# Kernel tuning notes

Hardware: AMD Instinct MI355X
Metric: run time of the kernel (lower is better)

The kernel has to match this reference:

```python
import jax, jax.numpy as jnp
import numpy as np
import math

H = 16
D_ATTN = 64
D_MID = 64
D_X = 1024
D_Z = 1024
D_OUT = 1024
B = 2
L_X = 2048
L_Z = 2048
MINUS_INFINITY = -1000000.0

def _xavier(key, shape):
    fan_in, fan_out = shape
    limit = math.sqrt(6.0 / (fan_in + fan_out))
    return jax.random.uniform(key, shape, jnp.float32, -limit, limit)

def setup_inputs() -> dict:
    key = jax.random.key(0)
    ks = jax.random.split(key, 8)
    primary = jax.random.normal(ks[0], (B, L_X, D_X), jnp.float32)
    context = jax.random.normal(ks[1], (B, L_Z, D_Z), jnp.float32)
    padding_mask = jnp.ones((B, L_Z), jnp.int32)
    # causal attention mask (b, l_x, l_z)
    attention_mask = jnp.broadcast_to(
        jnp.tril(jnp.ones((L_X, L_Z), jnp.int32))[None], (B, L_X, L_Z))
    W_qs = _xavier(ks[2], (D_X, H * D_ATTN))
    W_ks = _xavier(ks[3], (D_Z, H * D_ATTN))
    W_vs = _xavier(ks[4], (D_Z, H * D_MID))
    W_o = _xavier(ks[5], (H * D_MID, D_OUT))
    b_o = jnp.zeros((D_OUT,), jnp.float32)
    return {"primary": primary, "context": context,
            "padding_mask": padding_mask, "attention_mask": attention_mask,
            "W_qs": W_qs, "W_ks": W_ks, "W_vs": W_vs, "W_o": W_o, "b_o": b_o}

def reference(primary, context, padding_mask, attention_mask, W_qs, W_ks, W_vs, W_o, b_o):
    b, l_x, _ = primary.shape
    l_z = context.shape[1]
    # QKV projections, split into heads (head-major columns)
    q = (primary @ W_qs).reshape(b, l_x, H, D_ATTN).transpose(0, 2, 1, 3)  # (b,h,l_x,d_attn)
    k = (context @ W_ks).reshape(b, l_z, H, D_ATTN).transpose(0, 2, 1, 3)  # (b,h,l_z,d_attn)
    v = (context @ W_vs).reshape(b, l_z, H, D_MID).transpose(0, 2, 1, 3)   # (b,h,l_z,d_mid)
    scores = jnp.einsum('bhxd,bhzd->bhxz', q, k) / math.sqrt(D_ATTN)
    # combined mask: attention_mask AND padding_mask, broadcast over heads
    mask = (attention_mask * padding_mask[:, None, :])[:, None]  # (b,1,l_x,l_z)
    scores = jnp.where(mask == 0, MINUS_INFINITY, scores)
    attn = jax.nn.softmax(scores, axis=-1)
    out = jnp.einsum('bhxz,bhzm->bhxm', attn, v)  # (b,h,l_x,d_mid)
    out = out.transpose(0, 2, 1, 3).reshape(b, l_x, H * D_MID)
    return out @ W_o + b_o
```

## Files before the change

kernel.cpp:

```cpp
#include <hip/hip_runtime.h>

#define NB 2
#define LX 2048
#define LZ 2048
#define HH 16
#define DA 64
#define DM 64
#define HD 1024
#define MINF  -1000000.0f
#define QSC   0.1803368801f
#define DTHR  8.0f

typedef __attribute__((ext_vector_type(8))) short short8;
typedef __attribute__((ext_vector_type(4))) float f32x4;

static __device__ __forceinline__ ushort f2bf(float f) {
    union { float f; uint32_t u; } c; c.f = f;
    return (ushort)((c.u + 0x7FFFu + ((c.u >> 16) & 1u)) >> 16);
}

static __device__ __forceinline__ float bf2f(ushort u) {
    union { uint32_t u; float f; } c; c.u = (uint32_t)u << 16;
    return c.f;
}

static __device__ __forceinline__ uint32_t cvtpk(float lo, float hi) {
    uint32_t r;
    asm("v_cvt_pk_bf16_f32 %0, %1, %2" : "=v"(r) : "v"(lo), "v"(hi));
    return r;
}

#define GL16(g, l) __builtin_amdgcn_global_load_lds( \
    (const __attribute__((address_space(1))) void*)(g), \
    (__attribute__((address_space(3))) void*)(l), 16, 0, 0)

__global__ __launch_bounds__(256) void cvt_both(
    const float* __restrict__ pA, const float* __restrict__ pB,
    ushort* __restrict__ oA, ushort* __restrict__ oB)
{
    const int i = blockIdx.x * 256 + threadIdx.x;
    const float* in = (i < 1048576) ? pA : pB;
    ushort* out = (i < 1048576) ? oA : oB;
    const int j = i & 1048575;
    float4 v = ((const float4*)in)[j];
    ushort4 o;
    o.x = f2bf(v.x); o.y = f2bf(v.y); o.z = f2bf(v.z); o.w = f2bf(v.w);
    ((ushort4*)out)[j] = o;
}

__global__ __launch_bounds__(256) void wtrans4(
    const float* __restrict__ W0, const float* __restrict__ W1,
    const float* __restrict__ W2, const float* __restrict__ W3,
    ushort* __restrict__ T0, ushort* __restrict__ T1,
    ushort* __restrict__ T2, ushort* __restrict__ T3)
{
    const int zz = blockIdx.z;
    const float* W = (zz == 0) ? W0 : (zz == 1) ? W1 : (zz == 2) ? W2 : W3;
    ushort* Wt = (zz == 0) ? T0 : (zz == 1) ? T1 : (zz == 2) ? T2 : T3;

    __shared__ ushort Ls[64][72];
    const int n0 = blockIdx.x * 64, k0 = blockIdx.y * 64;
    const int t = threadIdx.x;
    const int rr = t >> 4, c4 = (t & 15) * 4;
    #pragma unroll
    for (int i = 0; i < 4; ++i) {
        const int r = rr + i * 16;
        float4 v = *(const float4*)&W[(size_t)(k0 + r) * 1024 + n0 + c4];
        Ls[c4 + 0][r] = f2bf(v.x);
        Ls[c4 + 1][r] = f2bf(v.y);
        Ls[c4 + 2][r] = f2bf(v.z);
        Ls[c4 + 3][r] = f2bf(v.w);
    }
    __syncthreads();
    const int n = t >> 2, kc = (t & 3) * 16;
    *(short8*)&Wt[(size_t)(n0 + n) * 1024 + k0 + kc]     = *(const short8*)&Ls[n][kc];
    *(short8*)&Wt[(size_t)(n0 + n) * 1024 + k0 + kc + 8] = *(const short8*)&Ls[n][kc + 8];
}

template <bool OUTF32>
static __device__ __forceinline__ void gemm_body(
    const ushort* __restrict__ A, const ushort* __restrict__ Bt,
    const float* __restrict__ bias, void* __restrict__ Cout, float osc)
{
    __shared__ ushort As[128 * 32];
    __shared__ ushort Bs[128 * 32];
    const int t = threadIdx.x;
    const int w = t >> 6, l = t & 63, lr = l & 15, lg = l >> 4;
    const int wr = w >> 1, wc = w & 1;
    const int n0 = blockIdx.x * 128, m0 = blockIdx.y * 128;

    const int c0 = t, c1 = t + 256;
    const ushort* a0 = &A[(size_t)(m0 + (c0 >> 2)) * 1024 + (c0 & 3) * 8];
    const ushort* a1 = &A[(size_t)(m0 + (c1 >> 2)) * 1024 + (c1 & 3) * 8];
    const ushort* b0 = &Bt[(size_t)(n0 + (c0 >> 2)) * 1024 + (c0 & 3) * 8];
    const ushort* b1 = &Bt[(size_t)(n0 + (c1 >> 2)) * 1024 + (c1 & 3) * 8];
    ushort* lA0 = &As[w * 512];
    ushort* lA1 = &As[(4 + w) * 512];
    ushort* lB0 = &Bs[w * 512];
    ushort* lB1 = &Bs[(4 + w) * 512];

    f32x4 acc[4][4];
    #pragma unroll
    for (int i = 0; i < 4; ++i)
        #pragma unroll
        for (int j = 0; j < 4; ++j) acc[i][j] = 0.f;

    for (int k0 = 0; k0 < 1024; k0 += 32) {
        __syncthreads();
        GL16(a0 + k0, lA0);
        GL16(a1 + k0, lA1);
        GL16(b0 + k0, lB0);
        GL16(b1 + k0, lB1);
        __syncthreads();
        short8 af[4], bf[4];
        #pragma unroll
        for (int mi = 0; mi < 4; ++mi)
            af[mi] = *(const short8*)&As[(wr * 64 + mi * 16 + lr) * 32 + lg * 8];
        #pragma unroll
        for (int nj = 0; nj < 4; ++nj)
            bf[nj] = *(const short8*)&Bs[(wc * 64 + nj * 16 + lr) * 32 + lg * 8];
        #pragma unroll
        for (int mi = 0; mi < 4; ++mi)
            #pragma unroll
            for (int nj = 0; nj < 4; ++nj)
                acc[mi][nj] = __builtin_amdgcn_mfma_f32_16x16x32_bf16(
                    af[mi], bf[nj], acc[mi][nj], 0, 0, 0);
    }

    const int row0 = m0 + wr * 64, col0 = n0 + wc * 64;
    #pragma unroll
    for (int mi = 0; mi < 4; ++mi)
        #pragma unroll
        for (int nj = 0; nj < 4; ++nj) {
            const int col = col0 + nj * 16 + lr;
            #pragma unroll
            for (int r = 0; r < 4; ++r) {
                const int row = row0 + mi * 16 + lg * 4 + r;
                const float v = acc[mi][nj][r];
                if (OUTF32)
                    ((float*)Cout)[(size_t)row * 1024 + col] = v + bias[col];
                else
                    ((ushort*)Cout)[(size_t)row * 1024 + col] = f2bf(v * osc);
            }
        }
}

__global__ __launch_bounds__(256) void gemm_qkv(
    const ushort* __restrict__ Pb, const ushort* __restrict__ Cb,
    const ushort* __restrict__ Wqt, const ushort* __restrict__ Wkt,
    const ushort* __restrict__ Wvt,
    ushort* __restrict__ Qb, ushort* __restrict__ Kb, ushort* __restrict__ Vb)
{
    const int z = blockIdx.z;
    const ushort* A  = (z == 0) ? Pb : Cb;
    const ushort* Bt = (z == 0) ? Wqt : (z == 1) ? Wkt : Wvt;
    ushort* C = (z == 0) ? Qb : (z == 1) ? Kb : Vb;
    const float osc = (z == 0) ? QSC : 1.0f;
    gemm_body<false>(A, Bt, nullptr, C, osc);
}

__global__ __launch_bounds__(256) void gemm_out(
    const ushort* __restrict__ A, const ushort* __restrict__ Bt,
    const float* __restrict__ bias, float* __restrict__ Cout)
{
    gemm_body<true>(A, Bt, bias, Cout, 1.0f);
}

__global__ __launch_bounds__(256) void mask_classify(
    const int* __restrict__ amask, const int* __restrict__ pmask,
    int* __restrict__ cls)
{
    const int bid = blockIdx.x;
    const int b = bid >> 10, xb = (bid >> 5) & 31, zb = bid & 31;
    const int t = threadIdx.x;
    int andv = 1, orv = 0;
    #pragma unroll
    for (int i = 0; i < 16; ++i) {
        const int e = t + i * 256;
        const int r = e >> 6, z = e & 63;
        const int m = amask[((size_t)b * LX + xb * 64 + r) * LZ + zb * 64 + z];
        const int p = pmask[(size_t)b * LZ + zb * 64 + z];
        const int v = (m != 0) & (p != 0);
        andv &= v; orv |= v;
    }
    __shared__ int sa[256];
    __shared__ int so[256];
    sa[t] = andv; so[t] = orv;
    __syncthreads();
    for (int s = 128; s > 0; s >>= 1) {
        if (t < s) { sa[t] &= sa[t + s]; so[t] |= so[t + s]; }
        __syncthreads();
    }
    if (t == 0) cls[bid] = so[0] ? (sa[0] ? 1 : 2) : 0;
}

__global__ __launch_bounds__(256, 4) void attn_mfma(
    const ushort* __restrict__ Qg, const ushort* __restrict__ Kg,
    const ushort* __restrict__ Vg, const int* __restrict__ amask,
    const int* __restrict__ pmask, const int* __restrict__ cls,
    ushort* __restrict__ Op, float2* __restrict__ ml)
{
    __shared__ ushort Ks[64 * 72];
    __shared__ ushort Vt[64 * 64];

    const int t = threadIdx.x, w = t >> 6, l = t & 63, lr = l & 15, lg = l >> 4;
    const int x = blockIdx.x, h = blockIdx.y;
    const int b = blockIdx.z >> 1, sKV = blockIdx.z & 1;
    const int fx = (x & 1) ? 31 - (x >> 1) : (x >> 1);
    const int qb = b ? 31 - fx : fx;
    const int qw = qb * 64 + w * 16;

    short8 qf[2];
    #pragma unroll
    for (int ks = 0; ks < 2; ++ks)
        qf[ks] = *(const short8*)&Qg[(size_t)(b * LX + qw + lr) * HD
                                     + h * DA + ks * 32 + lg * 8];

    float mrun = -1e30f, lrun = 0.f;
    f32x4 o[4];
    #pragma unroll
    for (int mj = 0; mj < 4; ++mj) o[mj] = 0.f;

    const int kz = t >> 2, kc = (t & 3) * 16;
    const int vz = (t >> 3) * 2, vc = (t & 7) * 8;

    for (int zb = sKV; zb < LZ / 64; zb += 2) {
        const int cl = cls[b * 1024 + qb * 32 + zb];
        if (cl == 0) continue;
        const int z0 = zb * 64;

        __syncthreads();
        {
            const ushort* kp = &Kg[(size_t)(b * LZ + z0 + kz) * HD + h * DA + kc];
            *(short8*)&Ks[kz * 72 + kc]     = *(const short8*)kp;
            *(short8*)&Ks[kz * 72 + kc + 8] = *(const short8*)(kp + 8);
            const ushort* vp = &Vg[(size_t)(b * LZ + z0 + vz) * HD + h * DM + vc];
            short8 v0 = *(const short8*)vp;
            short8 v1 = *(const short8*)(vp + HD);
            const int zc = vz >> 3, zo = vz & 7;
            #pragma unroll
            for (int j = 0; j < 8; ++j) {
                const int m = vc + j;
                const int idx = m * 64 + (((zc ^ m ^ (m >> 3)) & 7) << 3) + zo;
                const uint32_t pr = (uint32_t)(ushort)v0[j] | ((uint32_t)(ushort)v1[j] << 16);
                *(uint32_t*)&Vt[idx] = pr;
            }
        }
        __syncthreads();

        f32x4 s[4];
        __builtin_amdgcn_s_setprio(1);
        #pragma unroll
        for (int nj = 0; nj < 4; ++nj) {
            const short8 kf0 = *(const short8*)&Ks[(nj * 16 + lr) * 72 + lg * 8];
            const short8 kf1 = *(const short8*)&Ks[(nj * 16 + lr) * 72 + 32 + lg * 8];
            f32x4 z4 = 0.f;
            z4 = __builtin_amdgcn_mfma_f32_16x16x32_bf16(kf0, qf[0], z4, 0, 0, 0);
            z4 = __builtin_amdgcn_mfma_f32_16x16x32_bf16(kf1, qf[1], z4, 0, 0, 0);
            s[nj] = z4;
        }
        __builtin_amdgcn_s_setprio(0);
        if (cl == 2) {
            const size_t arow = (size_t)(b * LX + qw + lr) * LZ + z0;
            #pragma unroll
            for (int nj = 0; nj < 4; ++nj)
                #pragma unroll
                for (int r = 0; r < 4; ++r) {
                    const int z = nj * 16 + lg * 4 + r;
                    const int ok = (amask[arow + z] != 0) & (pmask[b * LZ + z0 + z] != 0);
                    if (!ok) s[nj][r] = MINF;
                }
        }
        {
            float pm = s[0][0];
            #pragma unroll
            for (int nj = 0; nj < 4; ++nj)
                #pragma unroll
                for (int r = 0; r < 4; ++r) pm = fmaxf(pm, s[nj][r]);
            pm = fmaxf(pm, __shfl_xor(pm, 16));
            pm = fmaxf(pm, __shfl_xor(pm, 32));
            if (__any(pm > mrun + DTHR)) {
                const float mn = fmaxf(mrun, pm);
                const float al = exp2f(mrun - mn);
                mrun = mn;
                lrun *= al;
                #pragma unroll
                for (int r = 0; r < 4; ++r) {
                    const float alq = __shfl(al, (lg << 2) + r);
                    #pragma unroll
                    for (int mj = 0; mj < 4; ++mj) o[mj][r] *= alq;
                }
            }
            #pragma unroll
            for (int nj = 0; nj < 4; ++nj)
                #pragma unroll
                for (int r = 0; r < 4; ++r) {
                    const float p = exp2f(s[nj][r] - mrun);
                    s[nj][r] = p;
                    lrun += p;
                }
        }
        short8 pa[2];
        {
            uint32_t pk01[4], pk23[4];
            #pragma unroll
            for (int nj = 0; nj < 4; ++nj) {
                pk01[nj] = cvtpk(s[nj][0], s[nj][1]);
                pk23[nj] = cvtpk(s[nj][2], s[nj][3]);
            }
            #pragma unroll
            for (int ks = 0; ks < 2; ++ks) {
                union { uint32_t d[4]; short8 v; } u;
                u.d[0] = pk01[2 * ks];
                u.d[1] = pk23[2 * ks];
                u.d[2] = pk01[2 * ks + 1];
                u.d[3] = pk23[2 * ks + 1];
                pa[ks] = u.v;
            }
        }
        __builtin_amdgcn_s_setprio(1);
        #pragma unroll
        for (int mj = 0; mj < 4; ++mj) {
            const int m_ = mj * 16 + lr;
            const int xr = (m_ ^ (m_ >> 3)) & 7;
            const int czb = lg >> 1;
            const int zo = (lg & 1) * 4;
            #pragma unroll
            for (int ks = 0; ks < 2; ++ks) {
                const int clo = (ks * 4 + czb) ^ xr;
                const int chi = (ks * 4 + 2 + czb) ^ xr;
                const uint2 lo = *(const uint2*)&Vt[m_ * 64 + ((clo & 7) << 3) + zo];
                const uint2 hi = *(const uint2*)&Vt[m_ * 64 + ((chi & 7) << 3) + zo];
                union { uint32_t d[4]; short8 v; } u;
                u.d[0] = lo.x; u.d[1] = lo.y; u.d[2] = hi.x; u.d[3] = hi.y;
                o[mj] = __builtin_amdgcn_mfma_f32_16x16x32_bf16(pa[ks], u.v, o[mj], 0, 0, 0);
            }
        }
        __builtin_amdgcn_s_setprio(0);
    }

    lrun += __shfl_xor(lrun, 16);
    lrun += __shfl_xor(lrun, 32);
    if (l < 16)
        ml[(size_t)((sKV * NB + b) * HH + h) * LX + qw + l] = make_float2(mrun, lrun);
    const size_t ob = (size_t)((sKV * NB + b) * LX + qw) * HD + h * DM;
    #pragma unroll
    for (int r = 0; r < 4; ++r)
        #pragma unroll
        for (int mj = 0; mj < 4; ++mj)
            Op[ob + (size_t)((lg << 2) + r) * HD + mj * 16 + lr] = f2bf(o[mj][r]);
}

__global__ __launch_bounds__(256) void attn_combine(
    const ushort* __restrict__ Op, const float2* __restrict__ ml,
    ushort* __restrict__ AOb)
{
    const int gid = blockIdx.x * 256 + threadIdx.x;
    if (gid >= NB * LX * HD / 8) return;
    const int row = gid >> 7;
    const int b = row >> 11, xx = row & 2047;
    const int h = (gid >> 3) & 15;
    const size_t e0 = (size_t)row * HD + (size_t)(gid & 127) * 8;
    const short8 p0 = *(const short8*)&Op[e0];
    const short8 p1 = *(const short8*)&Op[(size_t)NB * LX * HD + e0];
    const int mi = (b * HH + h) * LX + xx;
    const float2 a0 = ml[mi];
    const float2 a1 = ml[NB * HH * LX + mi];
    const float M = fmaxf(a0.x, a1.x);
    float w0 = exp2f(a0.x - M), w1 = exp2f(a1.x - M);
    const float inv = 1.f / (a0.y * w0 + a1.y * w1);
    w0 *= inv; w1 *= inv;
    short8 o;
    #pragma unroll
    for (int j = 0; j < 8; ++j)
        o[j] = (short)f2bf(bf2f((ushort)p0[j]) * w0 + bf2f((ushort)p1[j]) * w1);
    *(short8*)&AOb[e0] = o;
}

extern "C" void kernel_launch(void* const* d_in, const int* in_sizes, int n_in,
                              void* d_out, int out_size, void* d_ws, size_t ws_size,
                              hipStream_t stream)
{
    const float* primary = (const float*)d_in[0];
    const float* context = (const float*)d_in[1];
    const int*   pmask   = (const int*)d_in[2];
    const int*   amask   = (const int*)d_in[3];
    const float* Wq      = (const float*)d_in[4];
    const float* Wk      = (const float*)d_in[5];
    const float* Wv      = (const float*)d_in[6];
    const float* Wo      = (const float*)d_in[7];
    const float* bo      = (const float*)d_in[8];
    float* out = (float*)d_out;

    char* w8 = (char*)d_ws;
    ushort* Pb  = (ushort*)(w8 + 0);
    ushort* Cb  = (ushort*)(w8 + 8388608);
    ushort* Qb  = (ushort*)(w8 + 16777216);
    ushort* Kb  = (ushort*)(w8 + 25165824);
    ushort* Vb  = (ushort*)(w8 + 33554432);
    ushort* AOb = (ushort*)(w8 + 41943040);
    ushort* Wqt = (ushort*)(w8 + 50331648);
    ushort* Wkt = (ushort*)(w8 + 52428800);
    ushort* Wvt = (ushort*)(w8 + 54525952);
    ushort* Wot = (ushort*)(w8 + 56623104);
    int*    clsp = (int*)(w8 + 58720256);
    ushort* Op  = Pb;
    float2* mlp = (float2*)Wqt;

    cvt_both<<<8192, 256, 0, stream>>>(primary, context, Pb, Cb);
    wtrans4<<<dim3(16, 16, 4), 256, 0, stream>>>(Wq, Wk, Wv, Wo, Wqt, Wkt, Wvt, Wot);
    mask_classify<<<NB * 32 * 32, 256, 0, stream>>>(amask, pmask, clsp);
    gemm_qkv<<<dim3(8, 32, 3), 256, 0, stream>>>(Pb, Cb, Wqt, Wkt, Wvt, Qb, Kb, Vb);
    attn_mfma<<<dim3(32, 16, 4), 256, 0, stream>>>(Qb, Kb, Vb, amask, pmask, clsp, Op, mlp);
    attn_combine<<<2048, 256, 0, stream>>>(Op, mlp, AOb);
    gemm_out<<<dim3(8, 32), 256, 0, stream>>>(AOb, Wot, bo, out);
}
```

Measured before the change: 142.8 us.

## Prefetch next active KV tile into registers and remap blocks across XCDs

The attention kernel now reads the tile-class table once per wavefront via ballot to build bitmasks of active and mixed KV tiles. It then iterates only over active tiles, loading the next tile's K/V into registers while the current tile is computed, so global load latency overlaps with the MFMA work. Block indices are remapped so each XCD handles contiguous head/batch groups, aiming for better L2 reuse of K/V. Blocks with no active tiles write neutral partials and exit early, which is why the combine step now guards its divisor against zero.

```diff
diff --git a/kernel.cpp b/kernel.cpp
--- a/kernel.cpp
+++ b/kernel.cpp
@@ -204,11 +204,33 @@
     __shared__ ushort Vt[64 * 64];
 
     const int t = threadIdx.x, w = t >> 6, l = t & 63, lr = l & 15, lg = l >> 4;
-    const int x = blockIdx.x, h = blockIdx.y;
-    const int b = blockIdx.z >> 1, sKV = blockIdx.z & 1;
-    const int fx = (x & 1) ? 31 - (x >> 1) : (x >> 1);
+    const int flat = blockIdx.x + 32 * (blockIdx.y + 16 * blockIdx.z);
+    const int xcd = flat & 7, ii = flat >> 3;
+    const int g = xcd * 8 + (ii >> 5);
+    const int xr_ = ii & 31;
+    const int h = g & 15, bs = g >> 4;
+    const int b = bs & 1, sKV = bs >> 1;
+    const int fx = (xr_ & 1) ? 31 - (xr_ >> 1) : (xr_ >> 1);
     const int qb = b ? 31 - fx : fx;
     const int qw = qb * 64 + w * 16;
+
+    const uint32_t halfm = sKV ? 0xAAAAAAAAu : 0x55555555u;
+    const int cv = cls[b * 1024 + qb * 32 + (l & 31)];
+    const uint32_t act = (uint32_t)__ballot(cv != 0) & halfm;
+    const uint32_t mix = (uint32_t)__ballot(cv == 2) & halfm;
+
+    const size_t obase = (size_t)((sKV * NB + b) * LX + qw) * HD + h * DM;
+    if (act == 0) {
+        if (l < 16)
+            ml[(size_t)((sKV * NB + b) * HH + h) * LX + qw + l]
+                = make_float2(-1e30f, 0.f);
+        #pragma unroll
+        for (int r = 0; r < 4; ++r)
+            #pragma unroll
+            for (int mj = 0; mj < 4; ++mj)
+                Op[obase + (size_t)((lg << 2) + r) * HD + mj * 16 + lr] = 0;
+        return;
+    }
 
     short8 qf[2];
     #pragma unroll
@@ -224,29 +246,48 @@
     const int kz = t >> 2, kc = (t & 3) * 16;
     const int vz = (t >> 3) * 2, vc = (t & 7) * 8;
 
-    for (int zb = sKV; zb < LZ / 64; zb += 2) {
-        const int cl = cls[b * 1024 + qb * 32 + zb];
-        if (cl == 0) continue;
+    short8 kr0, kr1, vr0, vr1;
+
+#define PREFETCH(zbx) do {                                                     \
+        const int z0p = (zbx) * 64;                                           \
+        const ushort* kp = &Kg[(size_t)(b * LZ + z0p + kz) * HD + h * DA + kc];\
+        kr0 = *(const short8*)kp;                                             \
+        kr1 = *(const short8*)(kp + 8);                                       \
+        const ushort* vp = &Vg[(size_t)(b * LZ + z0p + vz) * HD + h * DM + vc];\
+        vr0 = *(const short8*)vp;                                             \
+        vr1 = *(const short8*)(vp + HD);                                      \
+    } while (0)
+
+#define WRITE_LDS() do {                                                       \
+        *(short8*)&Ks[kz * 72 + kc]     = kr0;                                \
+        *(short8*)&Ks[kz * 72 + kc + 8] = kr1;                                \
+        const int zc = vz >> 3, zo = vz & 7;                                  \
+        _Pragma("unroll")                                                      \
+        for (int j = 0; j < 8; ++j) {                                         \
+            const int m = vc + j;                                             \
+            const int idx = m * 64 + (((zc ^ m ^ (m >> 3)) & 7) << 3) + zo;   \
+            *(uint32_t*)&Vt[idx] =                                            \
+                (uint32_t)(ushort)vr0[j] | ((uint32_t)(ushort)vr1[j] << 16);  \
+        }                                                                      \
+    } while (0)
+
+    int zb = __builtin_ctz(act);
+    uint32_t rem = act & (act - 1);
+    PREFETCH(zb);
+
+    for (;;) {
+        __syncthreads();
+        WRITE_LDS();
+        __syncthreads();
+
+        const bool mixed = (mix >> zb) & 1;
         const int z0 = zb * 64;
-
-        __syncthreads();
-        {
-            const ushort* kp = &Kg[(size_t)(b * LZ + z0 + kz) * HD + h * DA + kc];
-            *(short8*)&Ks[kz * 72 + kc]     = *(const short8*)kp;
-            *(short8*)&Ks[kz * 72 + kc + 8] = *(const short8*)(kp + 8);
-            const ushort* vp = &Vg[(size_t)(b * LZ + z0 + vz) * HD + h * DM + vc];
-            short8 v0 = *(const short8*)vp;
-            short8 v1 = *(const short8*)(vp + HD);
-            const int zc = vz >> 3, zo = vz & 7;
-            #pragma unroll
-            for (int j = 0; j < 8; ++j) {
-                const int m = vc + j;
-                const int idx = m * 64 + (((zc ^ m ^ (m >> 3)) & 7) << 3) + zo;
-                const uint32_t pr = (uint32_t)(ushort)v0[j] | ((uint32_t)(ushort)v1[j] << 16);
-                *(uint32_t*)&Vt[idx] = pr;
-            }
-        }
-        __syncthreads();
+        int zbn = -1;
+        if (rem) {
+            zbn = __builtin_ctz(rem);
+            rem &= rem - 1;
+            PREFETCH(zbn);
+        }
 
         f32x4 s[4];
         __builtin_amdgcn_s_setprio(1);
@@ -260,7 +301,7 @@
             s[nj] = z4;
         }
         __builtin_amdgcn_s_setprio(0);
-        if (cl == 2) {
+        if (mixed) {
             const size_t arow = (size_t)(b * LX + qw + lr) * LZ + z0;
             #pragma unroll
             for (int nj = 0; nj < 4; ++nj)
@@ -337,18 +378,22 @@
             }
         }
         __builtin_amdgcn_s_setprio(0);
+
+        if (zbn < 0) break;
+        zb = zbn;
     }
 
     lrun += __shfl_xor(lrun, 16);
     lrun += __shfl_xor(lrun, 32);
     if (l < 16)
         ml[(size_t)((sKV * NB + b) * HH + h) * LX + qw + l] = make_float2(mrun, lrun);
-    const size_t ob = (size_t)((sKV * NB + b) * LX + qw) * HD + h * DM;
     #pragma unroll
     for (int r = 0; r < 4; ++r)
         #pragma unroll
         for (int mj = 0; mj < 4; ++mj)
-            Op[ob + (size_t)((lg << 2) + r) * HD + mj * 16 + lr] = f2bf(o[mj][r]);
+            Op[obase + (size_t)((lg << 2) + r) * HD + mj * 16 + lr] = f2bf(o[mj][r]);
+#undef PREFETCH
+#undef WRITE_LDS
 }
 
 __global__ __launch_bounds__(256) void attn_combine(
@@ -368,7 +413,7 @@
     const float2 a1 = ml[NB * HH * LX + mi];
     const float M = fmaxf(a0.x, a1.x);
     float w0 = exp2f(a0.x - M), w1 = exp2f(a1.x - M);
-    const float inv = 1.f / (a0.y * w0 + a1.y * w1);
+    const float inv = 1.f / fmaxf(a0.y * w0 + a1.y * w1, 1e-37f);
     w0 *= inv; w1 *= inv;
     short8 o;
     #pragma unroll
```

Measured after the change: 146.8 us. +2.8%, slower.

## Fuse prep kernels, merge K/V GEMM, remap attention blocks, fuse combine into out-proj

Applied to the files above, without the earlier changes.

The cast, weight-transpose and mask-classify kernels are merged into one launch. The K and V projections become a single 2048-wide GEMM that writes an interleaved KV buffer, using the fact that the transposed Wk and Wv sit next to each other in the workspace. Attention blocks are remapped so that heads and batches are grouped per XCD, for better cache locality. The split-KV combine is folded into the output GEMM's A-tile load, using a 64-row tile. This removes two launches and a full intermediate write and read pass, but the fused GEMM does the combine arithmetic inside its K-loop, uses smaller tiles, and has no prefetch of A.

```diff
diff --git a/kernel.cpp b/kernel.cpp
--- a/kernel.cpp
+++ b/kernel.cpp
@@ -7,6 +7,7 @@
 #define DA 64
 #define DM 64
 #define HD 1024
+#define KVS 2048
 #define MINF  -1000000.0f
 #define QSC   0.1803368801f
 #define DTHR  8.0f
@@ -34,60 +35,93 @@
     (const __attribute__((address_space(1))) void*)(g), \
     (__attribute__((address_space(3))) void*)(l), 16, 0, 0)
 
-__global__ __launch_bounds__(256) void cvt_both(
+__global__ __launch_bounds__(256) void prep(
     const float* __restrict__ pA, const float* __restrict__ pB,
-    ushort* __restrict__ oA, ushort* __restrict__ oB)
-{
-    const int i = blockIdx.x * 256 + threadIdx.x;
-    const float* in = (i < 1048576) ? pA : pB;
-    ushort* out = (i < 1048576) ? oA : oB;
-    const int j = i & 1048575;
-    float4 v = ((const float4*)in)[j];
-    ushort4 o;
-    o.x = f2bf(v.x); o.y = f2bf(v.y); o.z = f2bf(v.z); o.w = f2bf(v.w);
-    ((ushort4*)out)[j] = o;
-}
-
-__global__ __launch_bounds__(256) void wtrans4(
+    ushort* __restrict__ oA, ushort* __restrict__ oB,
     const float* __restrict__ W0, const float* __restrict__ W1,
     const float* __restrict__ W2, const float* __restrict__ W3,
     ushort* __restrict__ T0, ushort* __restrict__ T1,
-    ushort* __restrict__ T2, ushort* __restrict__ T3)
+    ushort* __restrict__ T2, ushort* __restrict__ T3,
+    const int* __restrict__ amask, const int* __restrict__ pmask,
+    int* __restrict__ cls)
 {
-    const int zz = blockIdx.z;
-    const float* W = (zz == 0) ? W0 : (zz == 1) ? W1 : (zz == 2) ? W2 : W3;
-    ushort* Wt = (zz == 0) ? T0 : (zz == 1) ? T1 : (zz == 2) ? T2 : T3;
-
-    __shared__ ushort Ls[64][72];
-    const int n0 = blockIdx.x * 64, k0 = blockIdx.y * 64;
+    const int fid = blockIdx.x;
     const int t = threadIdx.x;
-    const int rr = t >> 4, c4 = (t & 15) * 4;
-    #pragma unroll
-    for (int i = 0; i < 4; ++i) {
-        const int r = rr + i * 16;
-        float4 v = *(const float4*)&W[(size_t)(k0 + r) * 1024 + n0 + c4];
-        Ls[c4 + 0][r] = f2bf(v.x);
-        Ls[c4 + 1][r] = f2bf(v.y);
-        Ls[c4 + 2][r] = f2bf(v.z);
-        Ls[c4 + 3][r] = f2bf(v.w);
+    if (fid < 8192) {
+        const int i = fid * 256 + t;
+        const float* in = (i < 1048576) ? pA : pB;
+        ushort* out = (i < 1048576) ? oA : oB;
+        const int j = i & 1048575;
+        float4 v = ((const float4*)in)[j];
+        ushort4 o;
+        o.x = f2bf(v.x); o.y = f2bf(v.y); o.z = f2bf(v.z); o.w = f2bf(v.w);
+        ((ushort4*)out)[j] = o;
+    } else if (fid < 9216) {
+        __shared__ ushort Ls[64][72];
+        const int id2 = fid - 8192;
+        const int zz = id2 >> 8, rem = id2 & 255;
+        const float* W = (zz == 0) ? W0 : (zz == 1) ? W1 : (zz == 2) ? W2 : W3;
+        ushort* Wt = (zz == 0) ? T0 : (zz == 1) ? T1 : (zz == 2) ? T2 : T3;
+        const int n0 = (rem & 15) * 64, k0 = (rem >> 4) * 64;
+        const int rr = t >> 4, c4 = (t & 15) * 4;
+        #pragma unroll
+        for (int i = 0; i < 4; ++i) {
+            const int r = rr + i * 16;
+            float4 v = *(const float4*)&W[(size_t)(k0 + r) * 1024 + n0 + c4];
+            Ls[c4 + 0][r] = f2bf(v.x);
+            Ls[c4 + 1][r] = f2bf(v.y);
+            Ls[c4 + 2][r] = f2bf(v.z);
+            Ls[c4 + 3][r] = f2bf(v.w);
+        }
+        __syncthreads();
+        const int n = t >> 2, kc = (t & 3) * 16;
+        *(short8*)&Wt[(size_t)(n0 + n) * 1024 + k0 + kc]     = *(const short8*)&Ls[n][kc];
+        *(short8*)&Wt[(size_t)(n0 + n) * 1024 + k0 + kc + 8] = *(const short8*)&Ls[n][kc + 8];
+    } else {
+        const int bid = fid - 9216;
+        const int b = bid >> 10, xb = (bid >> 5) & 31, zb = bid & 31;
+        int andv = 1, orv = 0;
+        #pragma unroll
+        for (int i = 0; i < 16; ++i) {
+            const int e = t + i * 256;
+            const int r = e >> 6, z = e & 63;
+            const int m = amask[((size_t)b * LX + xb * 64 + r) * LZ + zb * 64 + z];
+            const int p = pmask[(size_t)b * LZ + zb * 64 + z];
+            const int v = (m != 0) & (p != 0);
+            andv &= v; orv |= v;
+        }
+        __shared__ int sa[256];
+        __shared__ int so[256];
+        sa[t] = andv; so[t] = orv;
+        __syncthreads();
+        for (int s = 128; s > 0; s >>= 1) {
+            if (t < s) { sa[t] &= sa[t + s]; so[t] |= so[t + s]; }
+            __syncthreads();
+        }
+        if (t == 0) cls[bid] = so[0] ? (sa[0] ? 1 : 2) : 0;
     }
-    __syncthreads();
-    const int n = t >> 2, kc = (t & 3) * 16;
-    *(short8*)&Wt[(size_t)(n0 + n) * 1024 + k0 + kc]     = *(const short8*)&Ls[n][kc];
-    *(short8*)&Wt[(size_t)(n0 + n) * 1024 + k0 + kc + 8] = *(const short8*)&Ls[n][kc + 8];
-}
-
-template <bool OUTF32>
-static __device__ __forceinline__ void gemm_body(
-    const ushort* __restrict__ A, const ushort* __restrict__ Bt,
-    const float* __restrict__ bias, void* __restrict__ Cout, float osc)
+}
+
+__global__ __launch_bounds__(256) void gemm_qkv(
+    const ushort* __restrict__ Pb, const ushort* __restrict__ Cb,
+    const ushort* __restrict__ Wqt, const ushort* __restrict__ Wkvt,
+    ushort* __restrict__ Qb, ushort* __restrict__ KV)
 {
+    const int bx = blockIdx.x;
+    const bool isQ = bx < 8;
+    const ushort* A  = isQ ? Pb : Cb;
+    const ushort* Bt = isQ ? Wqt : Wkvt;
+    ushort* Cout = isQ ? Qb : KV;
+    const int n0 = (isQ ? bx : bx - 8) * 128;
+    const int ostr = isQ ? 1024 : KVS;
+    const float osc = isQ ? QSC : 1.0f;
+
     __shared__ ushort As[128 * 32];
     __shared__ ushort Bs[128 * 32];
     const int t = threadIdx.x;
     const int w = t >> 6, l = t & 63, lr = l & 15, lg = l >> 4;
     const int wr = w >> 1, wc = w & 1;
-    const int n0 = blockIdx.x * 128, m0 = blockIdx.y * 128;
+    const int m0 = blockIdx.y * 128;
 
     const int c0 = t, c1 = t + 256;
     const ushort* a0 = &A[(size_t)(m0 + (c0 >> 2)) * 1024 + (c0 & 3) * 8];
@@ -136,77 +170,28 @@
             #pragma unroll
             for (int r = 0; r < 4; ++r) {
                 const int row = row0 + mi * 16 + lg * 4 + r;
-                const float v = acc[mi][nj][r];
-                if (OUTF32)
-                    ((float*)Cout)[(size_t)row * 1024 + col] = v + bias[col];
-                else
-                    ((ushort*)Cout)[(size_t)row * 1024 + col] = f2bf(v * osc);
-            }
-        }
-}
-
-__global__ __launch_bounds__(256) void gemm_qkv(
-    const ushort* __restrict__ Pb, const ushort* __restrict__ Cb,
-    const ushort* __restrict__ Wqt, const ushort* __restrict__ Wkt,
-    const ushort* __restrict__ Wvt,
-    ushort* __restrict__ Qb, ushort* __restrict__ Kb, ushort* __restrict__ Vb)
-{
-    const int z = blockIdx.z;
-    const ushort* A  = (z == 0) ? Pb : Cb;
-    const ushort* Bt = (z == 0) ? Wqt : (z == 1) ? Wkt : Wvt;
-    ushort* C = (z == 0) ? Qb : (z == 1) ? Kb : Vb;
-    const float osc = (z == 0) ? QSC : 1.0f;
-    gemm_body<false>(A, Bt, nullptr, C, osc);
-}
-
-__global__ __launch_bounds__(256) void gemm_out(
-    const ushort* __restrict__ A, const ushort* __restrict__ Bt,
-    const float* __restrict__ bias, float* __restrict__ Cout)
-{
-    gemm_body<true>(A, Bt, bias, Cout, 1.0f);
-}
-
-__global__ __launch_bounds__(256) void mask_classify(
+                Cout[(size_t)row * ostr + col] = f2bf(acc[mi][nj][r] * osc);
+            }
+        }
+}
+
+__global__ __launch_bounds__(256, 4) void attn_mfma(
+    const ushort* __restrict__ Qg, const ushort* __restrict__ KVg,
     const int* __restrict__ amask, const int* __restrict__ pmask,
-    int* __restrict__ cls)
-{
-    const int bid = blockIdx.x;
-    const int b = bid >> 10, xb = (bid >> 5) & 31, zb = bid & 31;
-    const int t = threadIdx.x;
-    int andv = 1, orv = 0;
-    #pragma unroll
-    for (int i = 0; i < 16; ++i) {
-        const int e = t + i * 256;
-        const int r = e >> 6, z = e & 63;
-        const int m = amask[((size_t)b * LX + xb * 64 + r) * LZ + zb * 64 + z];
-        const int p = pmask[(size_t)b * LZ + zb * 64 + z];
-        const int v = (m != 0) & (p != 0);
-        andv &= v; orv |= v;
-    }
-    __shared__ int sa[256];
-    __shared__ int so[256];
-    sa[t] = andv; so[t] = orv;
-    __syncthreads();
-    for (int s = 128; s > 0; s >>= 1) {
-        if (t < s) { sa[t] &= sa[t + s]; so[t] |= so[t + s]; }
-        __syncthreads();
-    }
-    if (t == 0) cls[bid] = so[0] ? (sa[0] ? 1 : 2) : 0;
-}
-
-__global__ __launch_bounds__(256, 4) void attn_mfma(
-    const ushort* __restrict__ Qg, const ushort* __restrict__ Kg,
-    const ushort* __restrict__ Vg, const int* __restrict__ amask,
-    const int* __restrict__ pmask, const int* __restrict__ cls,
-    ushort* __restrict__ Op, float2* __restrict__ ml)
+    const int* __restrict__ cls, ushort* __restrict__ Op,
+    float2* __restrict__ ml)
 {
     __shared__ ushort Ks[64 * 72];
     __shared__ ushort Vt[64 * 64];
 
     const int t = threadIdx.x, w = t >> 6, l = t & 63, lr = l & 15, lg = l >> 4;
-    const int x = blockIdx.x, h = blockIdx.y;
-    const int b = blockIdx.z >> 1, sKV = blockIdx.z & 1;
-    const int fx = (x & 1) ? 31 - (x >> 1) : (x >> 1);
+    const int flat = blockIdx.x + 32 * (blockIdx.y + 16 * blockIdx.z);
+    const int xcd = flat & 7, ii = flat >> 3;
+    const int g = xcd + 8 * (ii >> 5);
+    const int xr_ = ii & 31;
+    const int h = g & 15, bs = g >> 4;
+    const int b = bs & 1, sKV = bs >> 1;
+    const int fx = (xr_ & 1) ? 31 - (xr_ >> 1) : (xr_ >> 1);
     const int qb = b ? 31 - fx : fx;
     const int qw = qb * 64 + w * 16;
 
@@ -231,19 +216,19 @@
 
         __syncthreads();
         {
-            const ushort* kp = &Kg[(size_t)(b * LZ + z0 + kz) * HD + h * DA + kc];
+            const ushort* kp = &KVg[(size_t)(b * LZ + z0 + kz) * KVS + h * DA + kc];
             *(short8*)&Ks[kz * 72 + kc]     = *(const short8*)kp;
             *(short8*)&Ks[kz * 72 + kc + 8] = *(const short8*)(kp + 8);
-            const ushort* vp = &Vg[(size_t)(b * LZ + z0 + vz) * HD + h * DM + vc];
+            const ushort* vp = &KVg[(size_t)(b * LZ + z0 + vz) * KVS + 1024 + h * DM + vc];
             short8 v0 = *(const short8*)vp;
-            short8 v1 = *(const short8*)(vp + HD);
+            short8 v1 = *(const short8*)(vp + KVS);
             const int zc = vz >> 3, zo = vz & 7;
             #pragma unroll
             for (int j = 0; j < 8; ++j) {
                 const int m = vc + j;
                 const int idx = m * 64 + (((zc ^ m ^ (m >> 3)) & 7) << 3) + zo;
-                const uint32_t pr = (uint32_t)(ushort)v0[j] | ((uint32_t)(ushort)v1[j] << 16);
-                *(uint32_t*)&Vt[idx] = pr;
+                *(uint32_t*)&Vt[idx] =
+                    (uint32_t)(ushort)v0[j] | ((uint32_t)(ushort)v1[j] << 16);
             }
         }
         __syncthreads();
@@ -351,30 +336,90 @@
             Op[ob + (size_t)((lg << 2) + r) * HD + mj * 16 + lr] = f2bf(o[mj][r]);
 }
 
-__global__ __launch_bounds__(256) void attn_combine(
+__global__ __launch_bounds__(256) void gemm_out_fused(
     const ushort* __restrict__ Op, const float2* __restrict__ ml,
-    ushort* __restrict__ AOb)
+    const ushort* __restrict__ Bt, const float* __restrict__ bias,
+    float* __restrict__ Cout)
 {
-    const int gid = blockIdx.x * 256 + threadIdx.x;
-    if (gid >= NB * LX * HD / 8) return;
-    const int row = gid >> 7;
-    const int b = row >> 11, xx = row & 2047;
-    const int h = (gid >> 3) & 15;
-    const size_t e0 = (size_t)row * HD + (size_t)(gid & 127) * 8;
-    const short8 p0 = *(const short8*)&Op[e0];
-    const short8 p1 = *(const short8*)&Op[(size_t)NB * LX * HD + e0];
-    const int mi = (b * HH + h) * LX + xx;
-    const float2 a0 = ml[mi];
-    const float2 a1 = ml[NB * HH * LX + mi];
-    const float M = fmaxf(a0.x, a1.x);
-    float w0 = exp2f(a0.x - M), w1 = exp2f(a1.x - M);
-    const float inv = 1.f / (a0.y * w0 + a1.y * w1);
-    w0 *= inv; w1 *= inv;
-    short8 o;
-    #pragma unroll
-    for (int j = 0; j < 8; ++j)
-        o[j] = (short)f2bf(bf2f((ushort)p0[j]) * w0 + bf2f((ushort)p1[j]) * w1);
-    *(short8*)&AOb[e0] = o;
+    __shared__ ushort As[64 * 32];
+    __shared__ ushort Bs[128 * 32];
+    __shared__ float2 Wl[64][17];
+    const int t = threadIdx.x;
+    const int w = t >> 6, l = t & 63, lr = l & 15, lg = l >> 4;
+    const int wr = w >> 1, wc = w & 1;
+    const int n0 = blockIdx.x * 128, m0 = blockIdx.y * 64;
+
+    {
+        const int e = t * 4;
+        #pragma unroll
+        for (int j = 0; j < 4; ++j) {
+            const int rl = (e + j) >> 4, hh = (e + j) & 15;
+            const int ra = m0 + rl;
+            const int bb = ra >> 11, xx = ra & 2047;
+            const float2 a0 = ml[(size_t)(bb * HH + hh) * LX + xx];
+            const float2 a1 = ml[(size_t)((NB + bb) * HH + hh) * LX + xx];
+            const float M = fmaxf(a0.x, a1.x);
+            const float w0 = exp2f(a0.x - M), w1 = exp2f(a1.x - M);
+            const float inv = 1.f / fmaxf(a0.y * w0 + a1.y * w1, 1e-37f);
+            Wl[rl][hh] = make_float2(w0 * inv, w1 * inv);
+        }
+    }
+    __syncthreads();
+
+    const int ra = m0 + (t >> 2), ka = (t & 3) * 8;
+    const ushort* p0 = &Op[(size_t)ra * HD + ka];
+    const ushort* p1 = p0 + (size_t)NB * LX * HD;
+    const ushort* b0 = &Bt[(size_t)(n0 + (t >> 2)) * 1024 + ka];
+    const ushort* b1 = &Bt[(size_t)(n0 + 64 + (t >> 2)) * 1024 + ka];
+    ushort* lB0 = &Bs[w * 512];
+    ushort* lB1 = &Bs[(4 + w) * 512];
+
+    f32x4 acc[2][4];
+    #pragma unroll
+    for (int i = 0; i < 2; ++i)
+        #pragma unroll
+        for (int j = 0; j < 4; ++j) acc[i][j] = 0.f;
+
+    for (int k0 = 0; k0 < 1024; k0 += 32) {
+        const short8 q0 = *(const short8*)(p0 + k0);
+        const short8 q1 = *(const short8*)(p1 + k0);
+        const float2 wv = Wl[t >> 2][(k0 + ka) >> 6];
+        union { ushort d[8]; short8 v; } av;
+        #pragma unroll
+        for (int j = 0; j < 8; ++j)
+            av.d[j] = f2bf(bf2f((ushort)q0[j]) * wv.x + bf2f((ushort)q1[j]) * wv.y);
+        __syncthreads();
+        *(short8*)&As[t * 8] = av.v;
+        GL16(b0 + k0, lB0);
+        GL16(b1 + k0, lB1);
+        __syncthreads();
+        short8 af[2], bf[4];
+        #pragma unroll
+        for (int mi = 0; mi < 2; ++mi)
+            af[mi] = *(const short8*)&As[(wr * 32 + mi * 16 + lr) * 32 + lg * 8];
+        #pragma unroll
+        for (int nj = 0; nj < 4; ++nj)
+            bf[nj] = *(const short8*)&Bs[(wc * 64 + nj * 16 + lr) * 32 + lg * 8];
+        #pragma unroll
+        for (int mi = 0; mi < 2; ++mi)
+            #pragma unroll
+            for (int nj = 0; nj < 4; ++nj)
+                acc[mi][nj] = __builtin_amdgcn_mfma_f32_16x16x32_bf16(
+                    af[mi], bf[nj], acc[mi][nj], 0, 0, 0);
+    }
+
+    const int row0 = m0 + wr * 32, col0 = n0 + wc * 64;
+    #pragma unroll
+    for (int mi = 0; mi < 2; ++mi)
+        #pragma unroll
+        for (int nj = 0; nj < 4; ++nj) {
+            const int col = col0 + nj * 16 + lr;
+            #pragma unroll
+            for (int r = 0; r < 4; ++r) {
+                const int row = row0 + mi * 16 + lg * 4 + r;
+                Cout[(size_t)row * 1024 + col] = acc[mi][nj][r] + bias[col];
+            }
+        }
 }
 
 extern "C" void kernel_launch(void* const* d_in, const int* in_sizes, int n_in,
@@ -396,22 +441,19 @@
     ushort* Pb  = (ushort*)(w8 + 0);
     ushort* Cb  = (ushort*)(w8 + 8388608);
     ushort* Qb  = (ushort*)(w8 + 16777216);
-    ushort* Kb  = (ushort*)(w8 + 25165824);
-    ushort* Vb  = (ushort*)(w8 + 33554432);
-    ushort* AOb = (ushort*)(w8 + 41943040);
+    ushort* KV  = (ushort*)(w8 + 25165824);
     ushort* Wqt = (ushort*)(w8 + 50331648);
     ushort* Wkt = (ushort*)(w8 + 52428800);
     ushort* Wvt = (ushort*)(w8 + 54525952);
     ushort* Wot = (ushort*)(w8 + 56623104);
     int*    clsp = (int*)(w8 + 58720256);
-    ushort* Op  = Pb;
-    float2* mlp = (float2*)Wqt;
-
-    cvt_both<<<8192, 256, 0, stream>>>(primary, context, Pb, Cb);
-    wtrans4<<<dim3(16, 16, 4), 256, 0, stream>>>(Wq, Wk, Wv, Wo, Wqt, Wkt, Wvt, Wot);
-    mask_classify<<<NB * 32 * 32, 256, 0, stream>>>(amask, pmask, clsp);
-    gemm_qkv<<<dim3(8, 32, 3), 256, 0, stream>>>(Pb, Cb, Wqt, Wkt, Wvt, Qb, Kb, Vb);
-    attn_mfma<<<dim3(32, 16, 4), 256, 0, stream>>>(Qb, Kb, Vb, amask, pmask, clsp, Op, mlp);
-    attn_combine<<<2048, 256, 0, stream>>>(Op, mlp, AOb);
-    gemm_out<<<dim3(8, 32), 256, 0, stream>>>(AOb, Wot, bo, out);
-}
+    ushort* Op   = Pb;
+    float2* mlp  = (float2*)Wqt;
+
+    prep<<<11264, 256, 0, stream>>>(primary, context, Pb, Cb,
+                                    Wq, Wk, Wv, Wo, Wqt, Wkt, Wvt, Wot,
+                                    amask, pmask, clsp);
+    gemm_qkv<<<dim3(24, 32), 256, 0, stream>>>(Pb, Cb, Wqt, Wkt, Qb, KV);
+    attn_mfma<<<dim3(32, 16, 4), 256, 0, stream>>>(Qb, KV, amask, pmask, clsp, Op, mlp);
+    gemm_out_fused<<<dim3(8, 64), 256, 0, stream>>>(Op, mlp, Wot, bo, out);
+}
```

Result: faster. 134.9 us (-5.5%).
